# Optimization experiments

Measured on AMD Instinct MI355X. Metric: run time of the kernel, lower is better.

Reference implementation:

```python
import jax, jax.numpy as jnp
import numpy as np

B, I, O = 8192, 512, 512

def setup_inputs() -> dict:
    key = jax.random.key(0)
    k1, k2, k3, k4 = jax.random.split(key, 4)
    x = jax.random.normal(k1, (B, I), dtype=jnp.float32)
    # per-edge polynomial activation params: f_ij(t) = w1*t + w2*t^2 + w3*t^3 + b
    edge_w = jax.random.normal(k2, (I, O, 3), dtype=jnp.float32) * 0.1
    edge_b = jax.random.normal(k3, (I, O), dtype=jnp.float32) * 0.1
    # xavier-uniform combination weights
    limit = float(np.sqrt(6.0 / (I + O)))
    comb_w = jax.random.uniform(k4, (I, O), dtype=jnp.float32, minval=-limit, maxval=limit)
    return {"x": x, "edge_w": edge_w, "edge_b": edge_b, "comb_w": comb_w}

def reference(x, edge_w, edge_b, comb_w):
    # basis: [B, I, 3] = (t, t^2, t^3)
    basis = jnp.stack([x, x * x, x * x * x], axis=-1)
    # out[b,o] = sum_i comb_w[i,o] * (sum_k basis[b,i,k]*edge_w[i,o,k] + edge_b[i,o])
    # fused to avoid materializing [B, I, O]
    w_eff = edge_w * comb_w[:, :, None]            # [I, O, 3]
    out = jnp.einsum('bik,iok->bo', basis, w_eff)  # [B, O]
    out = out + jnp.sum(comb_w * edge_b, axis=0)   # bias term, [O]
    return out
```

## Files before the change

kernel.cpp:

```cpp
#include <hip/hip_runtime.h>
#include <hip/hip_bf16.h>
#include <stdint.h>


static constexpr int ON_ = 512;

typedef __bf16 bf16x8 __attribute__((ext_vector_type(8)));
typedef float  f32x4  __attribute__((ext_vector_type(4)));

__device__ __forceinline__ unsigned int f2bf(float f) {
    unsigned int u = __float_as_uint(f);
    return ((u + 0x7FFFu + ((u >> 16) & 1u)) >> 16);
}

__device__ __forceinline__ void nt_store4(uint4* p, uint4 v) {
    __builtin_nontemporal_store(v.x, &p->x);
    __builtin_nontemporal_store(v.y, &p->y);
    __builtin_nontemporal_store(v.z, &p->z);
    __builtin_nontemporal_store(v.w, &p->w);
}

__global__ __launch_bounds__(256) void pack_all(const float* __restrict__ x,
                                                const float* __restrict__ edge_w,
                                                const float* __restrict__ comb_w,
                                                const float* __restrict__ edge_b,
                                                uint4* __restrict__ Xpk,
                                                uint4* __restrict__ Bpk,
                                                float* __restrict__ bias_part) {
    __shared__ float xs[16 * 516];
    const int d = blockIdx.x;
    const int t = threadIdx.x;
    if (d < 512) {
        const int rb = (d & 7) * 64 + (d >> 3);
        const float* xb = x + (size_t)rb * 16 * 512;
#pragma unroll
        for (int it = 0; it < 8; ++it) {
            int e   = it * 1024 + t * 4;
            int row = e >> 9, col = e & 511;
            *(float4*)(xs + row * 516 + col) = *(const float4*)(xb + e);
        }
        __syncthreads();
        const int l = t & 63, wv = t >> 6;
        const float* src0 = xs + (l & 15) * 516 + ((l >> 4) << 3);
#pragma unroll
        for (int s = 0; s < 4; ++s) {
            const int g = wv * 4 + s;
            const float* src = src0 + g * 32;
            float4 v0 = *(const float4*)(src);
            float4 v1 = *(const float4*)(src + 4);
            uint4 o;
            o.x = f2bf(v0.x) | (f2bf(v0.y) << 16);
            o.y = f2bf(v0.z) | (f2bf(v0.w) << 16);
            o.z = f2bf(v1.x) | (f2bf(v1.y) << 16);
            o.w = f2bf(v1.z) | (f2bf(v1.w) << 16);
            Xpk[((size_t)rb * 16 + g) * 64 + l] = o;
        }
    } else if (d < 640) {
        int id = (d - 512) * 256 + t;
        int l  = id & 63;
        int u  = id >> 6;
        int g  = u & 15;
        int cb = u >> 4;
        int o  = cb * 16 + (l & 15);
        int i0 = g * 32 + ((l >> 4) << 3);
        unsigned int w[3][4];
#pragma unroll
        for (int j = 0; j < 4; ++j) {
            int ia = i0 + 2 * j, ic = ia + 1;
            float ca = comb_w[(size_t)ia * ON_ + o];
            float cc = comb_w[(size_t)ic * ON_ + o];
            const float* ea = edge_w + ((size_t)ia * ON_ + o) * 3;
            const float* ec = edge_w + ((size_t)ic * ON_ + o) * 3;
#pragma unroll
            for (int p = 0; p < 3; ++p)
                w[p][j] = f2bf(ea[p] * ca) | (f2bf(ec[p] * cc) << 16);
        }
        size_t base = ((size_t)cb * 48 + g * 3) * 64 + l;
        nt_store4(&Bpk[base],       make_uint4(w[0][0], w[0][1], w[0][2], w[0][3]));
        nt_store4(&Bpk[base + 64],  make_uint4(w[1][0], w[1][1], w[1][2], w[1][3]));
        nt_store4(&Bpk[base + 128], make_uint4(w[2][0], w[2][1], w[2][2], w[2][3]));
    } else {
        const int b  = d - 640;
        const int og = b >> 1, ih = b & 1;
        const int o  = og * 64 + (t & 63);
        const int s  = ih * 4 + (t >> 6);
        const int i0 = s * 64;
        float acc = 0.f;
#pragma unroll 8
        for (int i = i0; i < i0 + 64; ++i)
            acc += comb_w[(size_t)i * ON_ + o] * edge_b[(size_t)i * ON_ + o];
        __builtin_nontemporal_store(acc, &bias_part[s * ON_ + o]);
    }
}

#define STRIP(Am, MI, BP0, BP1, BP2, BQ0, BQ1, BQ2) do {                                   \
    bf16x8 a1_ = __builtin_bit_cast(bf16x8, Am);                                           \
    acc[MI][0] = __builtin_amdgcn_mfma_f32_16x16x32_bf16(a1_, __builtin_bit_cast(bf16x8, BP0), acc[MI][0], 0, 0, 0); \
    acc[MI][1] = __builtin_amdgcn_mfma_f32_16x16x32_bf16(a1_, __builtin_bit_cast(bf16x8, BQ0), acc[MI][1], 0, 0, 0); \
    float e0_ = __uint_as_float((Am).x << 16), e1_ = __uint_as_float((Am).x & 0xffff0000u); \
    float e2_ = __uint_as_float((Am).y << 16), e3_ = __uint_as_float((Am).y & 0xffff0000u); \
    float e4_ = __uint_as_float((Am).z << 16), e5_ = __uint_as_float((Am).z & 0xffff0000u); \
    float e6_ = __uint_as_float((Am).w << 16), e7_ = __uint_as_float((Am).w & 0xffff0000u); \
    float q0_ = e0_*e0_, q1_ = e1_*e1_, q2_ = e2_*e2_, q3_ = e3_*e3_;                      \
    float q4_ = e4_*e4_, q5_ = e5_*e5_, q6_ = e6_*e6_, q7_ = e7_*e7_;                      \
    bf16x8 s_ = (bf16x8){ (__bf16)q0_, (__bf16)q1_, (__bf16)q2_, (__bf16)q3_,              \
                          (__bf16)q4_, (__bf16)q5_, (__bf16)q6_, (__bf16)q7_ };            \
    acc[MI][0] = __builtin_amdgcn_mfma_f32_16x16x32_bf16(s_, __builtin_bit_cast(bf16x8, BP1), acc[MI][0], 0, 0, 0); \
    acc[MI][1] = __builtin_amdgcn_mfma_f32_16x16x32_bf16(s_, __builtin_bit_cast(bf16x8, BQ1), acc[MI][1], 0, 0, 0); \
    bf16x8 c_ = (bf16x8){ (__bf16)(q0_*e0_), (__bf16)(q1_*e1_), (__bf16)(q2_*e2_), (__bf16)(q3_*e3_), \
                          (__bf16)(q4_*e4_), (__bf16)(q5_*e5_), (__bf16)(q6_*e6_), (__bf16)(q7_*e7_) }; \
    acc[MI][0] = __builtin_amdgcn_mfma_f32_16x16x32_bf16(c_, __builtin_bit_cast(bf16x8, BP2), acc[MI][0], 0, 0, 0); \
    acc[MI][1] = __builtin_amdgcn_mfma_f32_16x16x32_bf16(c_, __builtin_bit_cast(bf16x8, BQ2), acc[MI][1], 0, 0, 0); \
} while (0)

#define COMP10(A0, A1, A2, A3, B0, B1, B2, B3, B4, B5) do {                                \
    STRIP(A0, 0, B0, B1, B2, B3, B4, B5);                                                  \
    STRIP(A1, 1, B0, B1, B2, B3, B4, B5);                                                  \
    STRIP(A2, 2, B0, B1, B2, B3, B4, B5);                                                  \
    STRIP(A3, 3, B0, B1, B2, B3, B4, B5);                                                  \
} while (0)

#define LOADG10(A0, A1, A2, A3, B0, B1, B2, B3, B4, B5) do {                               \
    A0 = *(const uint4*)(pa0); A1 = *(const uint4*)(pa1);                                  \
    A2 = *(const uint4*)(pa2); A3 = *(const uint4*)(pa3);                                  \
    B0 = *(const uint4*)(pb0);        B1 = *(const uint4*)(pb0 + 1024);                    \
    B2 = *(const uint4*)(pb0 + 2048); B3 = *(const uint4*)(pb1);                           \
    B4 = *(const uint4*)(pb1 + 1024); B5 = *(const uint4*)(pb1 + 2048);                    \
    pa0 += 1024; pa1 += 1024; pa2 += 1024; pa3 += 1024;                                    \
    pb0 += 3072; pb1 += 3072;                                                              \
} while (0)

#define WAITV(N) asm volatile("s_waitcnt vmcnt(" #N ")" ::: "memory")

__global__ __launch_bounds__(256, 2) void gemm_fused(const char* __restrict__ Xpk,
                                                     const char* __restrict__ Bpk,
                                                     const float* __restrict__ bias_part,
                                                     float* __restrict__ out) {
    const int tid = threadIdx.x;
    const int l   = tid & 63;
    const int wid = tid >> 6;
    const int wr  = wid >> 1, wc = wid & 1;

    int d  = blockIdx.x;
    int w  = (d & 7) * 64 + (d >> 3);
    int bx = w >> 3, by = w & 7;

    const char* pa0 = Xpk + ((size_t)(bx * 8 + wr * 4) * 16) * 1024 + (l << 4);
    const char* pa1 = pa0 + 16 * 1024;
    const char* pa2 = pa0 + 32 * 1024;
    const char* pa3 = pa0 + 48 * 1024;
    const char* pb0 = Bpk + ((size_t)(by * 4 + wc * 2) * 48) * 1024 + (l << 4);
    const char* pb1 = pb0 + 48 * 1024;

    f32x4 acc[4][2] = {};
    uint4 uA0, uA1, uA2, uA3, uB0, uB1, uB2, uB3, uB4, uB5;
    uint4 vA0, vA1, vA2, vA3, vB0, vB1, vB2, vB3, vB4, vB5;

    LOADG10(uA0, uA1, uA2, uA3, uB0, uB1, uB2, uB3, uB4, uB5);

#pragma unroll 1
    for (int it = 0; it < 8; ++it) {
        LOADG10(vA0, vA1, vA2, vA3, vB0, vB1, vB2, vB3, vB4, vB5);
        WAITV(10);
        COMP10(uA0, uA1, uA2, uA3, uB0, uB1, uB2, uB3, uB4, uB5);
        LOADG10(uA0, uA1, uA2, uA3, uB0, uB1, uB2, uB3, uB4, uB5);
        WAITV(10);
        COMP10(vA0, vA1, vA2, vA3, vB0, vB1, vB2, vB3, vB4, vB5);
    }

    int lr = l >> 4, lc = l & 15;
#pragma unroll
    for (int n = 0; n < 2; ++n) {
        int o = (by << 6) + (wc << 5) + (n << 4) + lc;
        float bv = 0.f;
#pragma unroll
        for (int k = 0; k < 8; ++k) bv += bias_part[k * ON_ + o];
#pragma unroll
        for (int m = 0; m < 4; ++m) {
            int r0 = (bx << 7) + (wr << 6) + (m << 4) + (lr << 2);
#pragma unroll
            for (int j = 0; j < 4; ++j)
                out[(size_t)(r0 + j) * ON_ + o] = acc[m][n][j] + bv;
        }
    }
}

extern "C" void kernel_launch(void* const* d_in, const int* in_sizes, int n_in,
                              void* d_out, int out_size, void* d_ws, size_t ws_size,
                              hipStream_t stream) {
    const float* x      = (const float*)d_in[0];
    const float* edge_w = (const float*)d_in[1];
    const float* edge_b = (const float*)d_in[2];
    const float* comb_w = (const float*)d_in[3];
    float* out = (float*)d_out;

    char* ws = (char*)d_ws;
    char* Xpk        = ws;
    char* Bpk        = ws + 8388608;
    float* bias_part = (float*)(ws + 8388608 + 1572864);

    hipLaunchKernelGGL(pack_all, dim3(512 + 128 + 16), dim3(256), 0, stream,
                       x, edge_w, comb_w, edge_b, (uint4*)Xpk, (uint4*)Bpk, bias_part);
    hipLaunchKernelGGL(gemm_fused, dim3(512), dim3(256), 0, stream, Xpk, Bpk, bias_part, out);
}
```

Measured before the change: 34.17 us.

## Read fp32 x directly in GEMM and drop the separate X packing pass

Removes the X-to-bf16 pre-pack stage. The GEMM now loads fp32 activations straight from x and converts them to bf16 in registers before the MFMA calls. This avoids writing and re-reading an 8 MB packed buffer and shrinks the pack kernel to the weight and bias work only. In exchange, the GEMM reads twice as many bytes for A, uses more VGPRs for in-flight float4 loads (14 outstanding per stage), and its row-strided loads are less contiguous than the packed layout.

```diff
diff --git a/kernel.cpp b/kernel.cpp
--- a/kernel.cpp
+++ b/kernel.cpp
@@ -20,43 +20,19 @@
     __builtin_nontemporal_store(v.w, &p->w);
 }
 
-__global__ __launch_bounds__(256) void pack_all(const float* __restrict__ x,
-                                                const float* __restrict__ edge_w,
-                                                const float* __restrict__ comb_w,
-                                                const float* __restrict__ edge_b,
-                                                uint4* __restrict__ Xpk,
-                                                uint4* __restrict__ Bpk,
-                                                float* __restrict__ bias_part) {
-    __shared__ float xs[16 * 516];
+__device__ __forceinline__ float4 mul4(float4 a, float4 b) {
+    return make_float4(a.x * b.x, a.y * b.y, a.z * b.z, a.w * b.w);
+}
+
+__global__ __launch_bounds__(256) void pack_bw(const float* __restrict__ edge_w,
+                                               const float* __restrict__ comb_w,
+                                               const float* __restrict__ edge_b,
+                                               uint4* __restrict__ Bpk,
+                                               float* __restrict__ bias_part) {
     const int d = blockIdx.x;
     const int t = threadIdx.x;
-    if (d < 512) {
-        const int rb = (d & 7) * 64 + (d >> 3);
-        const float* xb = x + (size_t)rb * 16 * 512;
-#pragma unroll
-        for (int it = 0; it < 8; ++it) {
-            int e   = it * 1024 + t * 4;
-            int row = e >> 9, col = e & 511;
-            *(float4*)(xs + row * 516 + col) = *(const float4*)(xb + e);
-        }
-        __syncthreads();
-        const int l = t & 63, wv = t >> 6;
-        const float* src0 = xs + (l & 15) * 516 + ((l >> 4) << 3);
-#pragma unroll
-        for (int s = 0; s < 4; ++s) {
-            const int g = wv * 4 + s;
-            const float* src = src0 + g * 32;
-            float4 v0 = *(const float4*)(src);
-            float4 v1 = *(const float4*)(src + 4);
-            uint4 o;
-            o.x = f2bf(v0.x) | (f2bf(v0.y) << 16);
-            o.y = f2bf(v0.z) | (f2bf(v0.w) << 16);
-            o.z = f2bf(v1.x) | (f2bf(v1.y) << 16);
-            o.w = f2bf(v1.z) | (f2bf(v1.w) << 16);
-            Xpk[((size_t)rb * 16 + g) * 64 + l] = o;
-        }
-    } else if (d < 640) {
-        int id = (d - 512) * 256 + t;
+    if (d < 128) {
+        int id = d * 256 + t;
         int l  = id & 63;
         int u  = id >> 6;
         int g  = u & 15;
@@ -80,7 +56,7 @@
         nt_store4(&Bpk[base + 64],  make_uint4(w[1][0], w[1][1], w[1][2], w[1][3]));
         nt_store4(&Bpk[base + 128], make_uint4(w[2][0], w[2][1], w[2][2], w[2][3]));
     } else {
-        const int b  = d - 640;
+        const int b  = d - 128;
         const int og = b >> 1, ih = b & 1;
         const int o  = og * 64 + (t & 63);
         const int s  = ih * 4 + (t >> 6);
@@ -93,46 +69,51 @@
     }
 }
 
-#define STRIP(Am, MI, BP0, BP1, BP2, BQ0, BQ1, BQ2) do {                                   \
-    bf16x8 a1_ = __builtin_bit_cast(bf16x8, Am);                                           \
-    acc[MI][0] = __builtin_amdgcn_mfma_f32_16x16x32_bf16(a1_, __builtin_bit_cast(bf16x8, BP0), acc[MI][0], 0, 0, 0); \
-    acc[MI][1] = __builtin_amdgcn_mfma_f32_16x16x32_bf16(a1_, __builtin_bit_cast(bf16x8, BQ0), acc[MI][1], 0, 0, 0); \
-    float e0_ = __uint_as_float((Am).x << 16), e1_ = __uint_as_float((Am).x & 0xffff0000u); \
-    float e2_ = __uint_as_float((Am).y << 16), e3_ = __uint_as_float((Am).y & 0xffff0000u); \
-    float e4_ = __uint_as_float((Am).z << 16), e5_ = __uint_as_float((Am).z & 0xffff0000u); \
-    float e6_ = __uint_as_float((Am).w << 16), e7_ = __uint_as_float((Am).w & 0xffff0000u); \
-    float q0_ = e0_*e0_, q1_ = e1_*e1_, q2_ = e2_*e2_, q3_ = e3_*e3_;                      \
-    float q4_ = e4_*e4_, q5_ = e5_*e5_, q6_ = e6_*e6_, q7_ = e7_*e7_;                      \
-    bf16x8 s_ = (bf16x8){ (__bf16)q0_, (__bf16)q1_, (__bf16)q2_, (__bf16)q3_,              \
-                          (__bf16)q4_, (__bf16)q5_, (__bf16)q6_, (__bf16)q7_ };            \
-    acc[MI][0] = __builtin_amdgcn_mfma_f32_16x16x32_bf16(s_, __builtin_bit_cast(bf16x8, BP1), acc[MI][0], 0, 0, 0); \
-    acc[MI][1] = __builtin_amdgcn_mfma_f32_16x16x32_bf16(s_, __builtin_bit_cast(bf16x8, BQ1), acc[MI][1], 0, 0, 0); \
-    bf16x8 c_ = (bf16x8){ (__bf16)(q0_*e0_), (__bf16)(q1_*e1_), (__bf16)(q2_*e2_), (__bf16)(q3_*e3_), \
-                          (__bf16)(q4_*e4_), (__bf16)(q5_*e5_), (__bf16)(q6_*e6_), (__bf16)(q7_*e7_) }; \
-    acc[MI][0] = __builtin_amdgcn_mfma_f32_16x16x32_bf16(c_, __builtin_bit_cast(bf16x8, BP2), acc[MI][0], 0, 0, 0); \
-    acc[MI][1] = __builtin_amdgcn_mfma_f32_16x16x32_bf16(c_, __builtin_bit_cast(bf16x8, BQ2), acc[MI][1], 0, 0, 0); \
+#define CVT8F(LO, HI) \
+    ((bf16x8){ (__bf16)(LO).x, (__bf16)(LO).y, (__bf16)(LO).z, (__bf16)(LO).w, \
+               (__bf16)(HI).x, (__bf16)(HI).y, (__bf16)(HI).z, (__bf16)(HI).w })
+
+#define STRIPF(MI, F0, F1, B0, B1, B2, B3, B4, B5) do {                                    \
+    bf16x8 a1_ = CVT8F(F0, F1);                                                            \
+    acc[MI][0] = __builtin_amdgcn_mfma_f32_16x16x32_bf16(a1_, __builtin_bit_cast(bf16x8, B0), acc[MI][0], 0, 0, 0); \
+    acc[MI][1] = __builtin_amdgcn_mfma_f32_16x16x32_bf16(a1_, __builtin_bit_cast(bf16x8, B3), acc[MI][1], 0, 0, 0); \
+    float4 q0_ = mul4(F0, F0), q1_ = mul4(F1, F1);                                         \
+    bf16x8 a2_ = CVT8F(q0_, q1_);                                                          \
+    acc[MI][0] = __builtin_amdgcn_mfma_f32_16x16x32_bf16(a2_, __builtin_bit_cast(bf16x8, B1), acc[MI][0], 0, 0, 0); \
+    acc[MI][1] = __builtin_amdgcn_mfma_f32_16x16x32_bf16(a2_, __builtin_bit_cast(bf16x8, B4), acc[MI][1], 0, 0, 0); \
+    float4 c0_ = mul4(q0_, F0), c1_ = mul4(q1_, F1);                                       \
+    bf16x8 a3_ = CVT8F(c0_, c1_);                                                          \
+    acc[MI][0] = __builtin_amdgcn_mfma_f32_16x16x32_bf16(a3_, __builtin_bit_cast(bf16x8, B2), acc[MI][0], 0, 0, 0); \
+    acc[MI][1] = __builtin_amdgcn_mfma_f32_16x16x32_bf16(a3_, __builtin_bit_cast(bf16x8, B5), acc[MI][1], 0, 0, 0); \
 } while (0)
 
-#define COMP10(A0, A1, A2, A3, B0, B1, B2, B3, B4, B5) do {                                \
-    STRIP(A0, 0, B0, B1, B2, B3, B4, B5);                                                  \
-    STRIP(A1, 1, B0, B1, B2, B3, B4, B5);                                                  \
-    STRIP(A2, 2, B0, B1, B2, B3, B4, B5);                                                  \
-    STRIP(A3, 3, B0, B1, B2, B3, B4, B5);                                                  \
+#define COMP14(F0a, F0b, F1a, F1b, F2a, F2b, F3a, F3b, B0, B1, B2, B3, B4, B5) do {        \
+    STRIPF(0, F0a, F0b, B0, B1, B2, B3, B4, B5);                                           \
+    STRIPF(1, F1a, F1b, B0, B1, B2, B3, B4, B5);                                           \
+    STRIPF(2, F2a, F2b, B0, B1, B2, B3, B4, B5);                                           \
+    STRIPF(3, F3a, F3b, B0, B1, B2, B3, B4, B5);                                           \
 } while (0)
 
-#define LOADG10(A0, A1, A2, A3, B0, B1, B2, B3, B4, B5) do {                               \
-    A0 = *(const uint4*)(pa0); A1 = *(const uint4*)(pa1);                                  \
-    A2 = *(const uint4*)(pa2); A3 = *(const uint4*)(pa3);                                  \
-    B0 = *(const uint4*)(pb0);        B1 = *(const uint4*)(pb0 + 1024);                    \
-    B2 = *(const uint4*)(pb0 + 2048); B3 = *(const uint4*)(pb1);                           \
-    B4 = *(const uint4*)(pb1 + 1024); B5 = *(const uint4*)(pb1 + 2048);                    \
-    pa0 += 1024; pa1 += 1024; pa2 += 1024; pa3 += 1024;                                    \
-    pb0 += 3072; pb1 += 3072;                                                              \
+#define LOADG14(G, F0a, F0b, F1a, F1b, F2a, F2b, F3a, F3b, B0, B1, B2, B3, B4, B5) do {    \
+    int gc_ = (G) < 16 ? (G) : 15;                                                         \
+    const float* a0_ = pa0 + gc_ * 32;                                                     \
+    const float* a1_ = pa1 + gc_ * 32;                                                     \
+    const float* a2_ = pa2 + gc_ * 32;                                                     \
+    const float* a3_ = pa3 + gc_ * 32;                                                     \
+    F0a = *(const float4*)(a0_); F0b = *(const float4*)(a0_ + 4);                          \
+    F1a = *(const float4*)(a1_); F1b = *(const float4*)(a1_ + 4);                          \
+    F2a = *(const float4*)(a2_); F2b = *(const float4*)(a2_ + 4);                          \
+    F3a = *(const float4*)(a3_); F3b = *(const float4*)(a3_ + 4);                          \
+    const char* b0_ = pb0 + (size_t)gc_ * 3072;                                            \
+    const char* b1_ = pb1 + (size_t)gc_ * 3072;                                            \
+    B0 = *(const uint4*)(b0_);        B1 = *(const uint4*)(b0_ + 1024);                    \
+    B2 = *(const uint4*)(b0_ + 2048); B3 = *(const uint4*)(b1_);                           \
+    B4 = *(const uint4*)(b1_ + 1024); B5 = *(const uint4*)(b1_ + 2048);                    \
 } while (0)
 
 #define WAITV(N) asm volatile("s_waitcnt vmcnt(" #N ")" ::: "memory")
 
-__global__ __launch_bounds__(256, 2) void gemm_fused(const char* __restrict__ Xpk,
+__global__ __launch_bounds__(256, 2) void gemm_fused(const float* __restrict__ x,
                                                      const char* __restrict__ Bpk,
                                                      const float* __restrict__ bias_part,
                                                      float* __restrict__ out) {
@@ -145,27 +126,29 @@
     int w  = (d & 7) * 64 + (d >> 3);
     int bx = w >> 3, by = w & 7;
 
-    const char* pa0 = Xpk + ((size_t)(bx * 8 + wr * 4) * 16) * 1024 + (l << 4);
-    const char* pa1 = pa0 + 16 * 1024;
-    const char* pa2 = pa0 + 32 * 1024;
-    const char* pa3 = pa0 + 48 * 1024;
-    const char* pb0 = Bpk + ((size_t)(by * 4 + wc * 2) * 48) * 1024 + (l << 4);
-    const char* pb1 = pb0 + 48 * 1024;
+    const float* pa0 = x + (size_t)(bx * 128 + wr * 64 + (l & 15)) * 512 + ((l >> 4) << 3);
+    const float* pa1 = pa0 + 16 * 512;
+    const float* pa2 = pa0 + 32 * 512;
+    const float* pa3 = pa0 + 48 * 512;
+    const char*  pb0 = Bpk + ((size_t)(by * 4 + wc * 2) * 48) * 1024 + (l << 4);
+    const char*  pb1 = pb0 + 48 * 1024;
 
     f32x4 acc[4][2] = {};
-    uint4 uA0, uA1, uA2, uA3, uB0, uB1, uB2, uB3, uB4, uB5;
-    uint4 vA0, vA1, vA2, vA3, vB0, vB1, vB2, vB3, vB4, vB5;
+    float4 uF0a, uF0b, uF1a, uF1b, uF2a, uF2b, uF3a, uF3b;
+    uint4  uB0, uB1, uB2, uB3, uB4, uB5;
+    float4 vF0a, vF0b, vF1a, vF1b, vF2a, vF2b, vF3a, vF3b;
+    uint4  vB0, vB1, vB2, vB3, vB4, vB5;
 
-    LOADG10(uA0, uA1, uA2, uA3, uB0, uB1, uB2, uB3, uB4, uB5);
+    LOADG14(0, uF0a, uF0b, uF1a, uF1b, uF2a, uF2b, uF3a, uF3b, uB0, uB1, uB2, uB3, uB4, uB5);
 
 #pragma unroll 1
     for (int it = 0; it < 8; ++it) {
-        LOADG10(vA0, vA1, vA2, vA3, vB0, vB1, vB2, vB3, vB4, vB5);
-        WAITV(10);
-        COMP10(uA0, uA1, uA2, uA3, uB0, uB1, uB2, uB3, uB4, uB5);
-        LOADG10(uA0, uA1, uA2, uA3, uB0, uB1, uB2, uB3, uB4, uB5);
-        WAITV(10);
-        COMP10(vA0, vA1, vA2, vA3, vB0, vB1, vB2, vB3, vB4, vB5);
+        LOADG14(2 * it + 1, vF0a, vF0b, vF1a, vF1b, vF2a, vF2b, vF3a, vF3b, vB0, vB1, vB2, vB3, vB4, vB5);
+        WAITV(14);
+        COMP14(uF0a, uF0b, uF1a, uF1b, uF2a, uF2b, uF3a, uF3b, uB0, uB1, uB2, uB3, uB4, uB5);
+        LOADG14(2 * it + 2, uF0a, uF0b, uF1a, uF1b, uF2a, uF2b, uF3a, uF3b, uB0, uB1, uB2, uB3, uB4, uB5);
+        WAITV(14);
+        COMP14(vF0a, vF0b, vF1a, vF1b, vF2a, vF2b, vF3a, vF3b, vB0, vB1, vB2, vB3, vB4, vB5);
     }
 
     int lr = l >> 4, lc = l & 15;
@@ -195,11 +178,10 @@
     float* out = (float*)d_out;
 
     char* ws = (char*)d_ws;
-    char* Xpk        = ws;
-    char* Bpk        = ws + 8388608;
-    float* bias_part = (float*)(ws + 8388608 + 1572864);
+    char* Bpk        = ws;
+    float* bias_part = (float*)(ws + 1572864);
 
-    hipLaunchKernelGGL(pack_all, dim3(512 + 128 + 16), dim3(256), 0, stream,
-                       x, edge_w, comb_w, edge_b, (uint4*)Xpk, (uint4*)Bpk, bias_part);
-    hipLaunchKernelGGL(gemm_fused, dim3(512), dim3(256), 0, stream, Xpk, Bpk, bias_part, out);
+    hipLaunchKernelGGL(pack_bw, dim3(144), dim3(256), 0, stream,
+                       edge_w, comb_w, edge_b, (uint4*)Bpk, bias_part);
+    hipLaunchKernelGGL(gemm_fused, dim3(512), dim3(256), 0, stream, x, Bpk, bias_part, out);
 }
```

After: 50.86 us. +48.9%, slower.
